# Kernel optimization log

Hardware: AMD Instinct MI355X
Metric: run time of the kernel (lower is better)

## Reference

```python
import jax, jax.numpy as jnp
import numpy as np

N = 50000   # nodes
E = 1600000 # edges
K = 5       # Chebyshev order
F_IN, H1, H2, P = 32, 32, 16, 12


def setup_inputs() -> dict:
    key = jax.random.key(0)
    ks = jax.random.split(key, 16)
    x = jax.random.normal(ks[0], (N, F_IN), dtype=jnp.float32)
    edge_index = jax.random.randint(ks[1], (2, E), 0, N, dtype=jnp.int64)
    edge_weight = jax.random.uniform(ks[2], (E,), dtype=jnp.float32)
    s = 0.1
    # Cell 1: 3 gates (z, r, h), each with x-conv [K,F_IN,H1] and h-conv [K,H1,H1]
    Wx1 = jax.random.normal(ks[3], (3, K, F_IN, H1), dtype=jnp.float32) * s
    bx1 = jax.random.normal(ks[4], (3, H1), dtype=jnp.float32) * s
    Wh1 = jax.random.normal(ks[5], (3, K, H1, H1), dtype=jnp.float32) * s
    bh1 = jax.random.normal(ks[6], (3, H1), dtype=jnp.float32) * s
    # Cell 2
    Wx2 = jax.random.normal(ks[7], (3, K, H1, H2), dtype=jnp.float32) * s
    bx2 = jax.random.normal(ks[8], (3, H2), dtype=jnp.float32) * s
    Wh2 = jax.random.normal(ks[9], (3, K, H2, H2), dtype=jnp.float32) * s
    bh2 = jax.random.normal(ks[10], (3, H2), dtype=jnp.float32) * s
    # Output linear (torch convention: weight [out,in])
    Wl = jax.random.normal(ks[11], (P, H2), dtype=jnp.float32) * s
    bl = jax.random.normal(ks[12], (P,), dtype=jnp.float32) * s
    return dict(x=x, edge_index=edge_index, edge_weight=edge_weight,
                Wx1=Wx1, bx1=bx1, Wh1=Wh1, bh1=bh1,
                Wx2=Wx2, bx2=bx2, Wh2=Wh2, bh2=bh2, Wl=Wl, bl=bl)


def _cheb_norm(edge_index, edge_weight):
    # ChebConv 'sym' norm with lambda_max=2: L_hat off-diagonal = -D^-1/2 A D^-1/2,
    # diagonal cancels to 0 (get_laplacian +1 self loop, add_self_loops fill -1).
    row, col = edge_index[0], edge_index[1]
    deg = jax.ops.segment_sum(edge_weight, row, num_segments=N)
    dis = jnp.where(deg > 0, jax.lax.rsqrt(jnp.maximum(deg, 1e-30)), 0.0)
    return -dis[row] * edge_weight * dis[col]


def _gconv_gru_forward(x, edge_index, edge_weight, Wx1, bx1, Wh1, bh1,
                       Wx2, bx2, Wh2, bh2, Wl, bl):
    row, col = edge_index[0], edge_index[1]
    wn = _cheb_norm(edge_index, edge_weight)

    def spmm(v):  # (L_hat @ v): gather source rows, scatter-add to targets
        return jax.ops.segment_sum(v[row] * wn[:, None], col, num_segments=N)

    def cheb(v, W, b):  # W: [K, Fin, Fout]
        Tx0 = v
        out = Tx0 @ W[0]
        Tx1 = spmm(Tx0)
        out = out + Tx1 @ W[1]
        for k in range(2, K):
            Tx2 = 2.0 * spmm(Tx1) - Tx0
            out = out + Tx2 @ W[k]
            Tx0, Tx1 = Tx1, Tx2
        return out + b

    def gru_cell(v, H, Wx, bx, Wh, bh):
        Z = jax.nn.sigmoid(cheb(v, Wx[0], bx[0]) + cheb(H, Wh[0], bh[0]))
        R = jax.nn.sigmoid(cheb(v, Wx[1], bx[1]) + cheb(H, Wh[1], bh[1]))
        Ht = jnp.tanh(cheb(v, Wx[2], bx[2]) + cheb(H * R, Wh[2], bh[2]))
        return Z * H + (1.0 - Z) * Ht

    h = gru_cell(x, jnp.zeros((N, H1), x.dtype), Wx1, bx1, Wh1, bh1)
    h = jax.nn.relu(h)  # dropout is identity in eval mode
    h = gru_cell(h, jnp.zeros((N, H2), x.dtype), Wx2, bx2, Wh2, bh2)
    h = jax.nn.relu(h)
    return h @ Wl.T + bl


def reference(x, edge_index, edge_weight, Wx1, bx1, Wh1, bh1,
              Wx2, bx2, Wh2, bh2, Wl, bl):
    return _gconv_gru_forward(x, edge_index, edge_weight, Wx1, bx1, Wh1, bh1,
                              Wx2, bx2, Wh2, bh2, Wl, bl)
```

## Files before the change

kernel.cpp:

```cpp
#include <hip/hip_runtime.h>
#include <math.h>

#define NN 50000
#define NE 1600000
#define KORD 5
#define NB 196
#define QTR 12500
#define GE 782
#define MT 64
#define NBK 1563
#define NBP 1600
#define NCH 256
#define ECH (NE / NCH)
#define EC4 (NE / 64)
#define PADE 1800192
#define CVB 1563

#define SCALE_W 2097152.0f
#define INV_SCALE_W (1.0f / 2097152.0f)
#define SCALE_D 4194304.0f
#define INV_SCALE_D (1.0f / 4194304.0f)

typedef _Float16 half8 __attribute__((ext_vector_type(8)));
typedef _Float16 half4v __attribute__((ext_vector_type(4)));
typedef float float4v __attribute__((ext_vector_type(4)));

__global__ __launch_bounds__(1024) void k_deg(const int* __restrict__ ei,
                                              const float* __restrict__ ew,
                                              int* __restrict__ deg_g) {
    __shared__ int h[QTR];
    int q = blockIdx.x >> 6, ch = blockIdx.x & 63;
    for (int i = threadIdx.x; i < QTR; i += 1024) h[i] = 0;
    __syncthreads();
    int base = ch * EC4, lo = q * QTR;
    for (int e = base + threadIdx.x; e < base + EC4; e += 1024) {
        int li = ei[e] - lo;
        if ((unsigned)li < (unsigned)QTR)
            atomicAdd(&h[li], __float2int_rn(ew[e] * SCALE_D));
    }
    __syncthreads();
    int* outp = deg_g + blockIdx.x * QTR;
    for (int i = threadIdx.x; i < QTR; i += 1024) outp[i] = h[i];
}

__global__ __launch_bounds__(256) void k_dis2cvt(const int* __restrict__ deg_g,
                                                 float* __restrict__ dis,
                                                 const float* __restrict__ x,
                                                 _Float16* __restrict__ x16) {
    int bid = blockIdx.x;
    if (bid < NB) {
        int n = bid * 256 + threadIdx.x;
        if (n >= NN) return;
        int q = n / QTR, i = n % QTR;
        const int* p = deg_g + (q * 64) * QTR + i;
        int s = 0;
#pragma unroll
        for (int c = 0; c < 64; c++) s += p[c * QTR];
        float d = (float)s * INV_SCALE_D;
        dis[n] = s > 0 ? rsqrtf(fmaxf(d, 1e-30f)) : 0.f;
    } else {
        int i = (bid - NB) * 256 + threadIdx.x;
        if (i < NN * 8) {
            float4 v = ((const float4*)x)[i];
            half4v h = {(_Float16)v.x, (_Float16)v.y, (_Float16)v.z, (_Float16)v.w};
            *(half4v*)(x16 + i * 4) = h;
        }
    }
}

__global__ __launch_bounds__(1024) void k_bhist(const int* __restrict__ ei,
                                                int* __restrict__ bh) {
    __shared__ int hist[NBK];
    int ch = blockIdx.x;
    for (int i = threadIdx.x; i < NBK; i += 1024) hist[i] = 0;
    __syncthreads();
    const int* cols = ei + NE;
    int base = ch * ECH;
    for (int e = base + threadIdx.x; e < base + ECH; e += 1024)
        atomicAdd(&hist[cols[e] >> 5], 1);
    __syncthreads();
    int* outp = bh + ch * NBP;
    for (int b = threadIdx.x; b < NBK; b += 1024) outp[b] = hist[b];
}

__global__ __launch_bounds__(256) void k_btot(const int* __restrict__ bh,
                                              int* __restrict__ tot) {
    int b = blockIdx.x * 256 + threadIdx.x;
    if (b >= NBP) return;
    int s = 0;
    if (b < NBK) {
#pragma unroll 8
        for (int ch = 0; ch < NCH; ch++) s += bh[ch * NBP + b];
    }
    tot[b] = s;
}

__global__ __launch_bounds__(1024) void k_bscan1(const int* __restrict__ tot,
                                                 int* __restrict__ off_bk) {
    __shared__ int s[1024];
    int t = threadIdx.x;
    int a0 = (2 * t < NBP) ? tot[2 * t] : 0;
    int a1 = (2 * t + 1 < NBP) ? tot[2 * t + 1] : 0;
    int p0 = (a0 + 127) & ~127;
    int p1 = (a1 + 127) & ~127;
    s[t] = p0 + p1;
    __syncthreads();
    for (int d = 1; d < 1024; d <<= 1) {
        int u = (t >= d) ? s[t - d] : 0;
        __syncthreads();
        s[t] += u;
        __syncthreads();
    }
    int excl = (t == 0) ? 0 : s[t - 1];
    if (2 * t < NBK) off_bk[2 * t] = excl;
    if (2 * t + 1 < NBK) off_bk[2 * t + 1] = excl + p0;
    if (t == 1023) off_bk[NBK] = s[1023];
}

__global__ __launch_bounds__(256) void k_curpad(int* __restrict__ bh,
                                                const int* __restrict__ off_bk,
                                                const int* __restrict__ tot,
                                                int2* __restrict__ edges) {
    int bid = blockIdx.x;
    if (bid < 7) {
        int b = bid * 256 + threadIdx.x;
        if (b >= NBK) return;
        int run = off_bk[b];
        for (int ch = 0; ch < NCH; ch++) {
            int v = bh[ch * NBP + b];
            bh[ch * NBP + b] = run;
            run += v;
        }
    } else {
        int b = bid - 7;
        int start = off_bk[b] + tot[b];
        int end = off_bk[b + 1];
        for (int i = start + threadIdx.x; i < end; i += 256)
            edges[i] = make_int2(0, 0);
    }
}

__global__ __launch_bounds__(1024) void k_cperm(const int* __restrict__ ei,
                                                const float* __restrict__ ew,
                                                const float* __restrict__ dis,
                                                const int* __restrict__ bh,
                                                int2* __restrict__ edges) {
    __shared__ int cur[NBK];
    int ch = blockIdx.x;
    const int* cp = bh + ch * NBP;
    for (int b = threadIdx.x; b < NBK; b += 1024) cur[b] = cp[b];
    __syncthreads();
    int base = ch * ECH;
    for (int e = base + threadIdx.x; e < base + ECH; e += 1024) {
        int r = ei[e], c = ei[NE + e];
        float w = -dis[r] * ew[e] * dis[c];
        int pos = atomicAdd(&cur[c >> 5], 1);
        int packed = (int)((unsigned)r | ((unsigned)(c & 31) << 16));
        edges[pos] = make_int2(packed, __float_as_int(w));
    }
}

#define SPMM_DS2(C0, W0, G0, C1, W1, G1)                       \
    {                                                          \
        int* a0 = &acc[C0][sub * 8];                           \
        int* a1 = &acc[C1][sub * 8];                           \
        atomicAdd(a0 + 0, __float2int_rn(W0 * (float)G0[0]));  \
        atomicAdd(a0 + 1, __float2int_rn(W0 * (float)G0[1]));  \
        atomicAdd(a0 + 2, __float2int_rn(W0 * (float)G0[2]));  \
        atomicAdd(a0 + 3, __float2int_rn(W0 * (float)G0[3]));  \
        atomicAdd(a0 + 4, __float2int_rn(W0 * (float)G0[4]));  \
        atomicAdd(a0 + 5, __float2int_rn(W0 * (float)G0[5]));  \
        atomicAdd(a0 + 6, __float2int_rn(W0 * (float)G0[6]));  \
        atomicAdd(a0 + 7, __float2int_rn(W0 * (float)G0[7]));  \
        atomicAdd(a1 + 0, __float2int_rn(W1 * (float)G1[0]));  \
        atomicAdd(a1 + 1, __float2int_rn(W1 * (float)G1[1]));  \
        atomicAdd(a1 + 2, __float2int_rn(W1 * (float)G1[2]));  \
        atomicAdd(a1 + 3, __float2int_rn(W1 * (float)G1[3]));  \
        atomicAdd(a1 + 4, __float2int_rn(W1 * (float)G1[4]));  \
        atomicAdd(a1 + 5, __float2int_rn(W1 * (float)G1[5]));  \
        atomicAdd(a1 + 6, __float2int_rn(W1 * (float)G1[6]));  \
        atomicAdd(a1 + 7, __float2int_rn(W1 * (float)G1[7]));  \
    }

__global__ __launch_bounds__(256) void k_spmm(const int* __restrict__ off_bk,
                                              const int2* __restrict__ edges,
                                              const _Float16* __restrict__ vin16,
                                              const float* __restrict__ prev,
                                              float* __restrict__ vout,
                                              _Float16* __restrict__ vout16,
                                              float scale) {
    __shared__ int acc[32][33];
    int b = blockIdx.x;
    {
        int nl = threadIdx.x >> 3, s4 = threadIdx.x & 7;
        int n = (b << 5) + nl;
        float4 p = make_float4(0.f, 0.f, 0.f, 0.f);
        if (prev && n < NN) p = ((const float4*)prev)[n * 8 + s4];
        int* a = &acc[nl][s4 * 4];
        a[0] = __float2int_rn(-p.x * SCALE_W);
        a[1] = __float2int_rn(-p.y * SCALE_W);
        a[2] = __float2int_rn(-p.z * SCALE_W);
        a[3] = __float2int_rn(-p.w * SCALE_W);
    }
    __syncthreads();
    int e0 = off_bk[b], e1 = off_bk[b + 1];
    int group = threadIdx.x >> 2, sub = threadIdx.x & 3;
    const half8* vin8 = (const half8*)vin16;
    float wscale = scale * SCALE_W;
    int i = e0 + group;
    if (i < e1) {
        int2 R0 = edges[i], R1 = edges[i + 64];
        half8 G0, G1;
        int C0 = 0, C1 = 0;
        float W0 = 0.f, W1 = 0.f;
        bool haveG = false;
        while (true) {
            int ni = i + 128;
            bool moreR = ni < e1;
            int2 N0, N1;
            if (moreR) {
                N0 = edges[ni]; N1 = edges[ni + 64];
            }
            half8 g0 = vin8[((unsigned)R0.x & 0xffffu) * 4 + sub];
            half8 g1 = vin8[((unsigned)R1.x & 0xffffu) * 4 + sub];
            if (haveG) SPMM_DS2(C0, W0, G0, C1, W1, G1);
            C0 = (unsigned)R0.x >> 16; C1 = (unsigned)R1.x >> 16;
            W0 = __int_as_float(R0.y) * wscale;
            W1 = __int_as_float(R1.y) * wscale;
            G0 = g0; G1 = g1;
            haveG = true;
            if (!moreR) break;
            R0 = N0; R1 = N1;
            i = ni;
        }
        SPMM_DS2(C0, W0, G0, C1, W1, G1);
    }
    __syncthreads();
    int base = b << 5;
    int nl = threadIdx.x >> 3, s4 = threadIdx.x & 7;
    int n = base + nl;
    if (n < NN) {
        const int* a = &acc[nl][s4 * 4];
        float4 o = make_float4((float)a[0] * INV_SCALE_W, (float)a[1] * INV_SCALE_W,
                               (float)a[2] * INV_SCALE_W, (float)a[3] * INV_SCALE_W);
        if (vout) ((float4*)vout)[n * 8 + s4] = o;
        half4v oh = {(_Float16)o.x, (_Float16)o.y, (_Float16)o.z, (_Float16)o.w};
        *(half4v*)(vout16 + n * 32 + s4 * 4) = oh;
    }
}

__global__ __launch_bounds__(256) void k_epi1(
    const _Float16* __restrict__ x16, const _Float16* __restrict__ t1,
    const _Float16* __restrict__ t2, const _Float16* __restrict__ t3,
    const _Float16* __restrict__ t4, const float* __restrict__ Wx1,
    const float* __restrict__ bx1, const float* __restrict__ bh1,
    float* __restrict__ h, _Float16* __restrict__ h16) {
    __shared__ _Float16 T[5][MT][40];
    __shared__ _Float16 Wt[64][168];
    int n0 = blockIdx.x * MT;
    const _Float16* bufs[5] = {x16, t1, t2, t3, t4};
#pragma unroll
    for (int b = 0; b < 5; b++) {
        for (int idx = threadIdx.x; idx < MT * 4; idx += 256) {
            int r = idx >> 2, c8 = idx & 3;
            int rr = n0 + r; if (rr >= NN) rr = NN - 1;
            half8 v = *(const half8*)(bufs[b] + rr * 32 + c8 * 8);
            *(half8*)&T[b][r][c8 * 8] = v;
        }
    }
    const float* Wz = Wx1;
    const float* Wh = Wx1 + 2 * KORD * 32 * 32;
    for (int idx = threadIdx.x; idx < 160 * 64; idx += 256) {
        int k = idx >> 6, n = idx & 63;
        int b = k >> 5, i = k & 31;
        float w = (n < 32) ? Wz[b * 1024 + i * 32 + n]
                           : Wh[b * 1024 + i * 32 + (n - 32)];
        Wt[n][k] = (_Float16)w;
    }
    __syncthreads();
    int wave = threadIdx.x >> 6;
    int lane = threadIdx.x & 63;
    int lo = lane & 15, quad = lane >> 4;
    float4v acc[4];
#pragma unroll
    for (int t = 0; t < 4; t++) acc[t] = (float4v){0.f, 0.f, 0.f, 0.f};
#pragma unroll
    for (int b = 0; b < 5; b++) {
        half8 a = *(half8*)&T[b][wave * 16 + lo][quad * 8];
#pragma unroll
        for (int t = 0; t < 4; t++) {
            half8 bf = *(half8*)&Wt[t * 16 + lo][b * 32 + quad * 8];
            acc[t] = __builtin_amdgcn_mfma_f32_16x16x32_f16(a, bf, acc[t], 0, 0, 0);
        }
    }
    int nd_base = n0 + wave * 16 + quad * 4;
#pragma unroll
    for (int t = 0; t < 2; t++) {
        int j = t * 16 + lo;
        float bz = bx1[j] + bh1[j];
        float bhb = bx1[64 + j] + bh1[64 + j];
#pragma unroll
        for (int reg = 0; reg < 4; reg++) {
            int nd = nd_base + reg;
            if (nd < NN) {
                float zz = acc[t][reg] + bz;
                float hh = acc[t + 2][reg] + bhb;
                float z = 1.f / (1.f + __expf(-zz));
                float tt = __expf(-2.f * fabsf(hh));
                float ht = copysignf((1.f - tt) / (1.f + tt), hh);
                float v = fmaxf((1.f - z) * ht, 0.f);
                h[nd * 32 + j] = v;
                h16[nd * 32 + j] = (_Float16)v;
            }
        }
    }
}

__global__ __launch_bounds__(256) void k_epi2(
    const _Float16* __restrict__ h16, const _Float16* __restrict__ t1,
    const _Float16* __restrict__ t2, const _Float16* __restrict__ t3,
    const _Float16* __restrict__ t4, const float* __restrict__ Wx2,
    const float* __restrict__ bx2, const float* __restrict__ bh2,
    const float* __restrict__ Wl, const float* __restrict__ bl,
    float* __restrict__ out) {
    __shared__ _Float16 T[5][MT][40];
    __shared__ _Float16 Wt[32][168];
    __shared__ float H2[MT][17];
    int n0 = blockIdx.x * MT;
    const _Float16* bufs[5] = {h16, t1, t2, t3, t4};
#pragma unroll
    for (int b = 0; b < 5; b++) {
        for (int idx = threadIdx.x; idx < MT * 4; idx += 256) {
            int r = idx >> 2, c8 = idx & 3;
            int rr = n0 + r; if (rr >= NN) rr = NN - 1;
            half8 v = *(const half8*)(bufs[b] + rr * 32 + c8 * 8);
            *(half8*)&T[b][r][c8 * 8] = v;
        }
    }
    const float* Wz = Wx2;
    const float* Wh = Wx2 + 2 * KORD * 32 * 16;
    for (int idx = threadIdx.x; idx < 160 * 32; idx += 256) {
        int k = idx >> 5, n = idx & 31;
        int b = k >> 5, i = k & 31;
        float w = (n < 16) ? Wz[b * 512 + i * 16 + n]
                           : Wh[b * 512 + i * 16 + (n - 16)];
        Wt[n][k] = (_Float16)w;
    }
    __syncthreads();
    int wave = threadIdx.x >> 6;
    int lane = threadIdx.x & 63;
    int lo = lane & 15, quad = lane >> 4;
    float4v acc[2];
    acc[0] = (float4v){0.f, 0.f, 0.f, 0.f};
    acc[1] = (float4v){0.f, 0.f, 0.f, 0.f};
#pragma unroll
    for (int b = 0; b < 5; b++) {
        half8 a = *(half8*)&T[b][wave * 16 + lo][quad * 8];
#pragma unroll
        for (int t = 0; t < 2; t++) {
            half8 bf = *(half8*)&Wt[t * 16 + lo][b * 32 + quad * 8];
            acc[t] = __builtin_amdgcn_mfma_f32_16x16x32_f16(a, bf, acc[t], 0, 0, 0);
        }
    }
    {
        int j = lo;
        float bz = bx2[j] + bh2[j];
        float bhb = bx2[32 + j] + bh2[32 + j];
        int ndl_base = wave * 16 + quad * 4;
#pragma unroll
        for (int reg = 0; reg < 4; reg++) {
            float zz = acc[0][reg] + bz;
            float hh = acc[1][reg] + bhb;
            float z = 1.f / (1.f + __expf(-zz));
            float tt = __expf(-2.f * fabsf(hh));
            float ht = copysignf((1.f - tt) / (1.f + tt), hh);
            H2[ndl_base + reg][j] = fmaxf((1.f - z) * ht, 0.f);
        }
    }
    __syncthreads();
    for (int idx = threadIdx.x; idx < MT * 12; idx += 256) {
        int n = idx / 12, p = idx % 12;
        int gn = n0 + n;
        if (gn < NN) {
            float o = bl[p];
#pragma unroll
            for (int jj = 0; jj < 16; jj++) o = fmaf(H2[n][jj], Wl[p * 16 + jj], o);
            out[gn * 12 + p] = o;
        }
    }
}


extern "C" void kernel_launch(void* const* d_in, const int* in_sizes, int n_in,
                              void* d_out, int out_size, void* d_ws, size_t ws_size,
                              hipStream_t stream) {
    const float* x   = (const float*)d_in[0];
    const int*   ei  = (const int*)d_in[1];
    const float* ew  = (const float*)d_in[2];
    const float* Wx1 = (const float*)d_in[3];
    const float* bx1 = (const float*)d_in[4];
    const float* bh1 = (const float*)d_in[6];
    const float* Wx2 = (const float*)d_in[7];
    const float* bx2 = (const float*)d_in[8];
    const float* bh2 = (const float*)d_in[10];
    const float* Wl  = (const float*)d_in[11];
    const float* bl  = (const float*)d_in[12];
    float* out = (float*)d_out;

    float* ws     = (float*)d_ws;
    float* dis    = ws;
    int*   bh     = (int*)(ws + 50048);
    int*   tot    = bh + NCH * NBP;
    int*   off_bk = tot + NBP;
    int2*  edges  = (int2*)(off_bk + NBP);
    float* T1     = (float*)(edges + PADE);
    float* T2     = T1 + NN * 32;
    float* T3     = T2 + NN * 32;
    float* hb     = T3 + NN * 32;
    _Float16* x16 = (_Float16*)(hb + NN * 32);
    _Float16* t1h = x16 + NN * 32;
    _Float16* t2h = t1h + NN * 32;
    _Float16* t3h = t2h + NN * 32;
    _Float16* t4h = t3h + NN * 32;
    _Float16* hbh = t4h + NN * 32;
    int*   deg_g  = (int*)T1;

    k_deg    <<<256, 1024, 0, stream>>>(ei, ew, deg_g);
    k_bhist  <<<NCH, 1024, 0, stream>>>(ei, bh);
    k_dis2cvt<<<NB + CVB, 256, 0, stream>>>(deg_g, dis, x, x16);
    k_btot   <<<7, 256, 0, stream>>>(bh, tot);
    k_bscan1 <<<1, 1024, 0, stream>>>(tot, off_bk);
    k_curpad <<<7 + NBK, 256, 0, stream>>>(bh, off_bk, tot, edges);
    k_cperm  <<<NCH, 1024, 0, stream>>>(ei, ew, dis, bh, edges);

    k_spmm<<<NBK, 256, 0, stream>>>(off_bk, edges, x16, nullptr, T1, t1h, 1.f);
    k_spmm<<<NBK, 256, 0, stream>>>(off_bk, edges, t1h, x,      T2, t2h, 2.f);
    k_spmm<<<NBK, 256, 0, stream>>>(off_bk, edges, t2h, T1,     T3, t3h, 2.f);
    k_spmm<<<NBK, 256, 0, stream>>>(off_bk, edges, t3h, T2, nullptr, t4h, 2.f);
    k_epi1<<<GE, 256, 0, stream>>>(x16, t1h, t2h, t3h, t4h, Wx1, bx1, bh1, hb, hbh);

    k_spmm<<<NBK, 256, 0, stream>>>(off_bk, edges, hbh, nullptr, T1, t1h, 1.f);
    k_spmm<<<NBK, 256, 0, stream>>>(off_bk, edges, t1h, hb,     T2, t2h, 2.f);
    k_spmm<<<NBK, 256, 0, stream>>>(off_bk, edges, t2h, T1,     T3, t3h, 2.f);
    k_spmm<<<NBK, 256, 0, stream>>>(off_bk, edges, t3h, T2, nullptr, t4h, 2.f);
    k_epi2<<<GE, 256, 0, stream>>>(hbh, t1h, t2h, t3h, t4h, Wx2, bx2, bh2, Wl, bl, out);
}
```

Before: 345.7 us.

## Merge preprocessing kernels, deepen SpMM edge prefetch, drop unused T3 fp32 writes

Fuses the degree and bucket-histogram kernels into one launch, and the bucket-total, dis and fp16 conversion kernels into another, cutting two launches and their serialization gaps. The SpMM inner loop now prefetches edges three iterations ahead and gathers two ahead, to hide gather latency better. It assumes the edge count per bucket is a multiple of 128, which the padded layout provides. The third Chebyshev SpMM no longer writes the fp32 T3 buffer, which nothing reads, saving write bandwidth. The deeper prefetch raises register pressure.

```diff
diff --git a/kernel.cpp b/kernel.cpp
--- a/kernel.cpp
+++ b/kernel.cpp
@@ -25,31 +25,57 @@
 typedef _Float16 half4v __attribute__((ext_vector_type(4)));
 typedef float float4v __attribute__((ext_vector_type(4)));
 
-__global__ __launch_bounds__(1024) void k_deg(const int* __restrict__ ei,
-                                              const float* __restrict__ ew,
-                                              int* __restrict__ deg_g) {
-    __shared__ int h[QTR];
-    int q = blockIdx.x >> 6, ch = blockIdx.x & 63;
-    for (int i = threadIdx.x; i < QTR; i += 1024) h[i] = 0;
-    __syncthreads();
-    int base = ch * EC4, lo = q * QTR;
-    for (int e = base + threadIdx.x; e < base + EC4; e += 1024) {
-        int li = ei[e] - lo;
-        if ((unsigned)li < (unsigned)QTR)
-            atomicAdd(&h[li], __float2int_rn(ew[e] * SCALE_D));
-    }
-    __syncthreads();
-    int* outp = deg_g + blockIdx.x * QTR;
-    for (int i = threadIdx.x; i < QTR; i += 1024) outp[i] = h[i];
-}
-
-__global__ __launch_bounds__(256) void k_dis2cvt(const int* __restrict__ deg_g,
-                                                 float* __restrict__ dis,
-                                                 const float* __restrict__ x,
-                                                 _Float16* __restrict__ x16) {
+__global__ __launch_bounds__(1024) void k_degbh(const int* __restrict__ ei,
+                                                const float* __restrict__ ew,
+                                                int* __restrict__ deg_g,
+                                                int* __restrict__ bh) {
+    __shared__ int sbuf[QTR];
     int bid = blockIdx.x;
-    if (bid < NB) {
-        int n = bid * 256 + threadIdx.x;
+    if (bid < 256) {
+        int q = bid >> 6, ch = bid & 63;
+        for (int i = threadIdx.x; i < QTR; i += 1024) sbuf[i] = 0;
+        __syncthreads();
+        int base = ch * EC4, lo = q * QTR;
+        for (int e = base + threadIdx.x; e < base + EC4; e += 1024) {
+            int li = ei[e] - lo;
+            if ((unsigned)li < (unsigned)QTR)
+                atomicAdd(&sbuf[li], __float2int_rn(ew[e] * SCALE_D));
+        }
+        __syncthreads();
+        int* outp = deg_g + bid * QTR;
+        for (int i = threadIdx.x; i < QTR; i += 1024) outp[i] = sbuf[i];
+    } else {
+        int ch = bid - 256;
+        for (int i = threadIdx.x; i < NBK; i += 1024) sbuf[i] = 0;
+        __syncthreads();
+        const int* cols = ei + NE;
+        int base = ch * ECH;
+        for (int e = base + threadIdx.x; e < base + ECH; e += 1024)
+            atomicAdd(&sbuf[cols[e] >> 5], 1);
+        __syncthreads();
+        int* outp = bh + ch * NBP;
+        for (int b = threadIdx.x; b < NBK; b += 1024) outp[b] = sbuf[b];
+    }
+}
+
+__global__ __launch_bounds__(256) void k_btotdiscvt(const int* __restrict__ bh,
+                                                    int* __restrict__ tot,
+                                                    const int* __restrict__ deg_g,
+                                                    float* __restrict__ dis,
+                                                    const float* __restrict__ x,
+                                                    _Float16* __restrict__ x16) {
+    int bid = blockIdx.x;
+    if (bid < 7) {
+        int b = bid * 256 + threadIdx.x;
+        if (b >= NBP) return;
+        int s = 0;
+        if (b < NBK) {
+#pragma unroll 8
+            for (int ch = 0; ch < NCH; ch++) s += bh[ch * NBP + b];
+        }
+        tot[b] = s;
+    } else if (bid < 7 + NB) {
+        int n = (bid - 7) * 256 + threadIdx.x;
         if (n >= NN) return;
         int q = n / QTR, i = n % QTR;
         const int* p = deg_g + (q * 64) * QTR + i;
@@ -59,40 +85,13 @@
         float d = (float)s * INV_SCALE_D;
         dis[n] = s > 0 ? rsqrtf(fmaxf(d, 1e-30f)) : 0.f;
     } else {
-        int i = (bid - NB) * 256 + threadIdx.x;
+        int i = (bid - 7 - NB) * 256 + threadIdx.x;
         if (i < NN * 8) {
             float4 v = ((const float4*)x)[i];
             half4v h = {(_Float16)v.x, (_Float16)v.y, (_Float16)v.z, (_Float16)v.w};
             *(half4v*)(x16 + i * 4) = h;
         }
     }
-}
-
-__global__ __launch_bounds__(1024) void k_bhist(const int* __restrict__ ei,
-                                                int* __restrict__ bh) {
-    __shared__ int hist[NBK];
-    int ch = blockIdx.x;
-    for (int i = threadIdx.x; i < NBK; i += 1024) hist[i] = 0;
-    __syncthreads();
-    const int* cols = ei + NE;
-    int base = ch * ECH;
-    for (int e = base + threadIdx.x; e < base + ECH; e += 1024)
-        atomicAdd(&hist[cols[e] >> 5], 1);
-    __syncthreads();
-    int* outp = bh + ch * NBP;
-    for (int b = threadIdx.x; b < NBK; b += 1024) outp[b] = hist[b];
-}
-
-__global__ __launch_bounds__(256) void k_btot(const int* __restrict__ bh,
-                                              int* __restrict__ tot) {
-    int b = blockIdx.x * 256 + threadIdx.x;
-    if (b >= NBP) return;
-    int s = 0;
-    if (b < NBK) {
-#pragma unroll 8
-        for (int ch = 0; ch < NCH; ch++) s += bh[ch * NBP + b];
-    }
-    tot[b] = s;
 }
 
 __global__ __launch_bounds__(1024) void k_bscan1(const int* __restrict__ tot,
@@ -207,33 +206,37 @@
     int group = threadIdx.x >> 2, sub = threadIdx.x & 3;
     const half8* vin8 = (const half8*)vin16;
     float wscale = scale * SCALE_W;
-    int i = e0 + group;
-    if (i < e1) {
-        int2 R0 = edges[i], R1 = edges[i + 64];
-        half8 G0, G1;
-        int C0 = 0, C1 = 0;
-        float W0 = 0.f, W1 = 0.f;
-        bool haveG = false;
-        while (true) {
-            int ni = i + 128;
-            bool moreR = ni < e1;
-            int2 N0, N1;
-            if (moreR) {
-                N0 = edges[ni]; N1 = edges[ni + 64];
+    int nit = (e1 - e0) >> 7;
+    if (nit > 0) {
+        int i = e0 + group;
+        int2 Ra0 = edges[i], Ra1 = edges[i + 64];
+        int2 Rb0 = make_int2(0, 0), Rb1 = make_int2(0, 0);
+        int2 Rc0 = make_int2(0, 0), Rc1 = make_int2(0, 0);
+        if (nit > 1) { Rb0 = edges[i + 128]; Rb1 = edges[i + 192]; }
+        if (nit > 2) { Rc0 = edges[i + 256]; Rc1 = edges[i + 320]; }
+        half8 Ga0 = vin8[((unsigned)Ra0.x & 0xffffu) * 4 + sub];
+        half8 Ga1 = vin8[((unsigned)Ra1.x & 0xffffu) * 4 + sub];
+        half8 Gb0 = {}, Gb1 = {};
+        if (nit > 1) {
+            Gb0 = vin8[((unsigned)Rb0.x & 0xffffu) * 4 + sub];
+            Gb1 = vin8[((unsigned)Rb1.x & 0xffffu) * 4 + sub];
+        }
+        for (int k = 0; k < nit; k++) {
+            int2 Rd0 = make_int2(0, 0), Rd1 = make_int2(0, 0);
+            if (k + 3 < nit) { Rd0 = edges[i + 384]; Rd1 = edges[i + 448]; }
+            half8 Gc0 = {}, Gc1 = {};
+            if (k + 2 < nit) {
+                Gc0 = vin8[((unsigned)Rc0.x & 0xffffu) * 4 + sub];
+                Gc1 = vin8[((unsigned)Rc1.x & 0xffffu) * 4 + sub];
             }
-            half8 g0 = vin8[((unsigned)R0.x & 0xffffu) * 4 + sub];
-            half8 g1 = vin8[((unsigned)R1.x & 0xffffu) * 4 + sub];
-            if (haveG) SPMM_DS2(C0, W0, G0, C1, W1, G1);
-            C0 = (unsigned)R0.x >> 16; C1 = (unsigned)R1.x >> 16;
-            W0 = __int_as_float(R0.y) * wscale;
-            W1 = __int_as_float(R1.y) * wscale;
-            G0 = g0; G1 = g1;
-            haveG = true;
-            if (!moreR) break;
-            R0 = N0; R1 = N1;
-            i = ni;
-        }
-        SPMM_DS2(C0, W0, G0, C1, W1, G1);
+            int C0 = (unsigned)Ra0.x >> 16, C1 = (unsigned)Ra1.x >> 16;
+            float W0 = __int_as_float(Ra0.y) * wscale;
+            float W1 = __int_as_float(Ra1.y) * wscale;
+            SPMM_DS2(C0, W0, Ga0, C1, W1, Ga1);
+            Ra0 = Rb0; Ra1 = Rb1; Rb0 = Rc0; Rb1 = Rc1; Rc0 = Rd0; Rc1 = Rd1;
+            Ga0 = Gb0; Ga1 = Gb1; Gb0 = Gc0; Gb1 = Gc1;
+            i += 128;
+        }
     }
     __syncthreads();
     int base = b << 5;
@@ -425,23 +428,21 @@
     _Float16* hbh = t4h + NN * 32;
     int*   deg_g  = (int*)T1;
 
-    k_deg    <<<256, 1024, 0, stream>>>(ei, ew, deg_g);
-    k_bhist  <<<NCH, 1024, 0, stream>>>(ei, bh);
-    k_dis2cvt<<<NB + CVB, 256, 0, stream>>>(deg_g, dis, x, x16);
-    k_btot   <<<7, 256, 0, stream>>>(bh, tot);
-    k_bscan1 <<<1, 1024, 0, stream>>>(tot, off_bk);
-    k_curpad <<<7 + NBK, 256, 0, stream>>>(bh, off_bk, tot, edges);
-    k_cperm  <<<NCH, 1024, 0, stream>>>(ei, ew, dis, bh, edges);
+    k_degbh     <<<512, 1024, 0, stream>>>(ei, ew, deg_g, bh);
+    k_btotdiscvt<<<7 + NB + CVB, 256, 0, stream>>>(bh, tot, deg_g, dis, x, x16);
+    k_bscan1    <<<1, 1024, 0, stream>>>(tot, off_bk);
+    k_curpad    <<<7 + NBK, 256, 0, stream>>>(bh, off_bk, tot, edges);
+    k_cperm     <<<NCH, 1024, 0, stream>>>(ei, ew, dis, bh, edges);
 
     k_spmm<<<NBK, 256, 0, stream>>>(off_bk, edges, x16, nullptr, T1, t1h, 1.f);
     k_spmm<<<NBK, 256, 0, stream>>>(off_bk, edges, t1h, x,      T2, t2h, 2.f);
-    k_spmm<<<NBK, 256, 0, stream>>>(off_bk, edges, t2h, T1,     T3, t3h, 2.f);
+    k_spmm<<<NBK, 256, 0, stream>>>(off_bk, edges, t2h, T1, nullptr, t3h, 2.f);
     k_spmm<<<NBK, 256, 0, stream>>>(off_bk, edges, t3h, T2, nullptr, t4h, 2.f);
     k_epi1<<<GE, 256, 0, stream>>>(x16, t1h, t2h, t3h, t4h, Wx1, bx1, bh1, hb, hbh);
 
     k_spmm<<<NBK, 256, 0, stream>>>(off_bk, edges, hbh, nullptr, T1, t1h, 1.f);
     k_spmm<<<NBK, 256, 0, stream>>>(off_bk, edges, t1h, hb,     T2, t2h, 2.f);
-    k_spmm<<<NBK, 256, 0, stream>>>(off_bk, edges, t2h, T1,     T3, t3h, 2.f);
+    k_spmm<<<NBK, 256, 0, stream>>>(off_bk, edges, t2h, T1, nullptr, t3h, 2.f);
     k_spmm<<<NBK, 256, 0, stream>>>(off_bk, edges, t3h, T2, nullptr, t4h, 2.f);
     k_epi2<<<GE, 256, 0, stream>>>(hbh, t1h, t2h, t3h, t4h, Wx2, bx2, bh2, Wl, bl, out);
 }
```

Result: no change. 340.0 us (median of 2 runs) (-1.7%).
